# Optimization experiments

Measured on AMD Instinct MI355X. Metric: run time of the kernel, lower is better.

Reference implementation:

```python
import jax, jax.numpy as jnp
import numpy as np

UNITS = 1024
INPUT_SIZE = 1024


def setup_inputs() -> dict:
    key = jax.random.key(0)
    k1, k2, k3 = jax.random.split(key, 3)
    T, B = 512, 64
    inputs = jax.random.normal(k1, (T, B, INPUT_SIZE), dtype=jnp.float32)
    # xavier_uniform for kernel
    limit = float(np.sqrt(6.0 / (INPUT_SIZE + 4 * UNITS)))
    kernel = jax.random.uniform(k2, (INPUT_SIZE, 4 * UNITS), dtype=jnp.float32,
                                minval=-limit, maxval=limit)
    # orthogonal init for recurrent_kernel
    a = jax.random.normal(k3, (4 * UNITS, UNITS), dtype=jnp.float32)
    q, r = jnp.linalg.qr(a)
    q = q * jnp.sign(jnp.diagonal(r))[None, :]
    recurrent_kernel = q.T.astype(jnp.float32)  # [UNITS, 4*UNITS]
    bias = jnp.zeros((4 * UNITS,), dtype=jnp.float32)
    return {"inputs": inputs, "kernel": kernel,
            "recurrent_kernel": recurrent_kernel, "bias": bias}


def _lstm(inputs, kernel, recurrent_kernel, bias):
    T, B, _ = inputs.shape
    U = recurrent_kernel.shape[0]
    # Precompute input projection for all timesteps (same math, one big GEMM)
    xz = jnp.einsum('tbi,ij->tbj', inputs, kernel) + bias  # [T, B, 4U]

    def step(carry, xz_t):
        ht, ct = carry
        z = xz_t + ht @ recurrent_kernel  # [B, 4U]
        z_i, z_f, z_c, z_o = jnp.split(z, 4, axis=1)
        i = jax.nn.sigmoid(z_i)
        f = jax.nn.sigmoid(z_f)
        c_tilde = jnp.tanh(z_c)
        o = jax.nn.sigmoid(z_o)
        ct = f * ct + i * c_tilde
        ht = o * jnp.tanh(ct)
        return (ht, ct), ht

    h0 = jnp.zeros((B, U), dtype=inputs.dtype)
    c0 = jnp.zeros((B, U), dtype=inputs.dtype)
    (ht, ct), outputs = jax.lax.scan(step, (h0, c0), xz)
    return outputs, (ht, ct)


def reference(inputs, kernel, recurrent_kernel, bias):
    return _lstm(inputs, kernel, recurrent_kernel, bias)
```

## Files before the change

### kernel.cpp

```cpp
#include <hip/hip_runtime.h>

typedef __attribute__((ext_vector_type(8))) short short8;
typedef __attribute__((ext_vector_type(4))) float floatx4;
typedef __attribute__((ext_vector_type(4))) int intx4;

#define T_STEPS 512
#define OUT_HT_OFF 33554432ull
#define OUT_CT_OFF 33619968ull

#define WXH_OFF  0ull
#define WXL_OFF  (8ull << 20)
#define HBUF_OFF (16ull << 20)
#define BAR_OFF  ((16ull << 20) + (512ull << 10))
#define WS_NEED  ((16ull << 20) + (512ull << 10) + 4096ull)


static __device__ __forceinline__ unsigned short bf16_rne(float f) {
    union { float f; unsigned int u; } v; v.f = f;
    return (unsigned short)((v.u + 0x7FFFu + ((v.u >> 16) & 1u)) >> 16);
}
static __device__ __forceinline__ float bf16f(unsigned short u) {
    union { unsigned int u; float f; } v; v.u = ((unsigned int)u) << 16;
    return v.f;
}

__global__ void ws_sentinel(float* out) { out[threadIdx.x] = 2.0f; }

__global__ void __launch_bounds__(256) wsplit(const float* __restrict__ W,
                                              unsigned short* __restrict__ wxh,
                                              unsigned short* __restrict__ wxl) {
    __shared__ float tile[64][65];
    const int tx = threadIdx.x & 63;
    const int ty = threadIdx.x >> 6;
    const int cb = blockIdx.x * 64;
    const int kb = blockIdx.y * 64;
    #pragma unroll
    for (int i = 0; i < 16; ++i) {
        int kl = i * 4 + ty;
        tile[kl][tx] = W[(size_t)(kb + kl) * 4096 + cb + tx];
    }
    __syncthreads();
    #pragma unroll
    for (int i = 0; i < 16; ++i) {
        int cl = i * 4 + ty;
        float v = tile[tx][cl];
        unsigned short hi = bf16_rne(v);
        unsigned short lo = bf16_rne(v - bf16f(hi));
        wxh[(size_t)(cb + cl) * 1024 + kb + tx] = hi;
        wxl[(size_t)(cb + cl) * 1024 + kb + tx] = lo;
    }
}

#define HLOAD(dst, OFF) \
    asm volatile("global_load_dwordx4 %0, %1, off offset:" OFF " sc0 sc1" \
                 : "=v"(dst) : "v"(hp8) : "memory");

#define HSTAGE(q, ra, rb, WAITSTR) \
    asm volatile("s_waitcnt " WAITSTR ::: "memory"); \
    __builtin_amdgcn_sched_barrier(0); \
    { unsigned w0=(unsigned)(ra).x, w1=(unsigned)(ra).y, w2=(unsigned)(ra).z, w3=(unsigned)(ra).w; \
      unsigned v0=(unsigned)(rb).x, v1=(unsigned)(rb).y, v2=(unsigned)(rb).z, v3=(unsigned)(rb).w; \
      intx4 hh, ll; \
      hh.x=(int)((w0&0xffffu)|(w1<<16)); hh.y=(int)((w2&0xffffu)|(w3<<16)); \
      hh.z=(int)((v0&0xffffu)|(v1<<16)); hh.w=(int)((v2&0xffffu)|(v3<<16)); \
      ll.x=(int)((w0>>16)|(w1&0xffff0000u)); ll.y=(int)((w2>>16)|(w3&0xffff0000u)); \
      ll.z=(int)((v0>>16)|(v1&0xffff0000u)); ll.w=(int)((v2>>16)|(v3&0xffff0000u)); \
      *(intx4*)(AhH + (wave*8+(q))*1024 + lane*16) = hh; \
      *(intx4*)(AhL + (wave*8+(q))*1024 + lane*16) = ll; }

__global__ void __launch_bounds__(256, 1) lstm_scan(
    const float* __restrict__ R,
    const float* __restrict__ bias,
    const float* __restrict__ x,
    const unsigned short* __restrict__ wxh,
    const unsigned short* __restrict__ wxl,
    unsigned* __restrict__ hbuf,
    unsigned* __restrict__ bar,
    float* __restrict__ out)
{
    __shared__ __align__(16) char AxH[32768];
    __shared__ __align__(16) char AxL[32768];
    __shared__ __align__(16) char AhH[32768];
    __shared__ __align__(16) char AhL[32768];
    __shared__ float zxl[1024];
    __shared__ unsigned s_as[2];

    const int tid  = threadIdx.x;
    const int lane = tid & 63;
    const int wave = tid >> 6;

    if (tid == 0) {
        unsigned xcc;
        asm volatile("s_getreg_b32 %0, hwreg(HW_REG_XCC_ID)" : "=s"(xcc));
        xcc &= 7u;
        unsigned slot = __hip_atomic_fetch_add(bar + 640 + xcc * 32, 1u,
                            __ATOMIC_RELAXED, __HIP_MEMORY_SCOPE_AGENT);
        s_as[0] = xcc; s_as[1] = slot;
    }
    __syncthreads();
    const int xcd  = (int)s_as[0];
    const int slot = (int)(s_as[1] & 31u);
    const int rg   = slot >> 3;
    const int jg   = xcd * 8 + (slot & 7);

    const int rowbase = rg * 16;
    const int c16  = lane & 15;
    const int kgrp = lane >> 4;
    const int gate = c16 >> 2;
    const int jj   = c16 & 3;
    const int mycol = gate * 1024 + jg * 16 + wave * 4 + jj;

    short8 rh[32], rl[32];
    #pragma unroll
    for (int kk = 0; kk < 32; ++kk) {
        int kb = kk * 32 + kgrp * 8;
        short8 h8, l8;
        #pragma unroll
        for (int j = 0; j < 8; ++j) {
            float v = R[(size_t)(kb + j) * 4096 + mycol];
            unsigned short hh = bf16_rne(v);
            h8[j] = (short)hh;
            l8[j] = (short)bf16_rne(v - bf16f(hh));
        }
        rh[kk] = h8; rl[kk] = l8;
    }
    const float biasreg = bias[mycol];

    const int erow  = tid >> 4;
    const int eunit = tid & 15;
    const int ew    = eunit >> 2;
    const int ejj   = eunit & 3;
    const int grow  = rowbase + erow;
    const int gcol  = jg * 16 + eunit;
    const size_t cidx = (size_t)grow * 1024 + gcol;
    float c_state = 0.f;

    const int srow = rowbase + c16;
    const int skof = kgrp * 8;

    const unsigned short* bph = wxh + (size_t)mycol * 1024 + kgrp * 8;
    const unsigned short* bpl = wxl + (size_t)mycol * 1024 + kgrp * 8;

    floatx4 zxcur;
    {
        #pragma unroll
        for (int q = 0; q < 8; ++q) {
            int kc = wave * 8 + q;
            const float* src = x + (size_t)srow * 1024 + kc * 32 + skof;
            floatx4 f0 = *(const floatx4*)src;
            floatx4 f1 = *(const floatx4*)(src + 4);
            short8 h8, l8;
            #pragma unroll
            for (int j = 0; j < 4; ++j) {
                unsigned short q0 = bf16_rne(f0[j]);
                unsigned short q1 = bf16_rne(f1[j]);
                h8[j] = (short)q0; h8[j + 4] = (short)q1;
                l8[j] = (short)bf16_rne(f0[j] - bf16f(q0));
                l8[j + 4] = (short)bf16_rne(f1[j] - bf16f(q1));
            }
            *(short8*)(AxH + kc * 1024 + lane * 16) = h8;
            *(short8*)(AxL + kc * 1024 + lane * 16) = l8;
        }
        __syncthreads();
        floatx4 b0 = {0,0,0,0}, b1 = {0,0,0,0}, b2 = {0,0,0,0}, b3 = {0,0,0,0};
        #pragma unroll
        for (int kk = 0; kk < 32; ++kk) {
            short8 bxh = *(const short8*)(bph + kk * 32);
            short8 bxl = *(const short8*)(bpl + kk * 32);
            short8 axh = *(const short8*)(AxH + kk * 1024 + lane * 16);
            short8 axl = *(const short8*)(AxL + kk * 1024 + lane * 16);
            b0 = __builtin_amdgcn_mfma_f32_16x16x32_bf16(axh, bxh, b0, 0, 0, 0);
            b1 = __builtin_amdgcn_mfma_f32_16x16x32_bf16(axh, bxl, b1, 0, 0, 0);
            b2 = __builtin_amdgcn_mfma_f32_16x16x32_bf16(axl, bxh, b2, 0, 0, 0);
            b3 = __builtin_amdgcn_mfma_f32_16x16x32_bf16(axl, bxl, b3, 0, 0, 0);
        }
        #pragma unroll
        for (int i = 0; i < 4; ++i)
            zxcur[i] = ((b0[i] + b1[i]) + (b2[i] + b3[i])) + biasreg;
        __syncthreads();
    }

    for (int t = 0; t < T_STEPS; ++t) {
        const bool more = (t + 1 < T_STEPS);

        if (t > 0) {
            const char* hp8 = (const char*)(hbuf + (size_t)(t & 1) * 65536)
                            + srow * 4096 + wave * 1024 + kgrp * 32;
            intx4 r0, r1, r2, r3, r4, r5, r6, r7;
            intx4 r8, r9, r10, r11, r12, r13, r14, r15;
            HLOAD(r0,  "0")   HLOAD(r1,  "16")
            HLOAD(r2,  "128") HLOAD(r3,  "144")
            HLOAD(r4,  "256") HLOAD(r5,  "272")
            HLOAD(r6,  "384") HLOAD(r7,  "400")
            HLOAD(r8,  "512") HLOAD(r9,  "528")
            HLOAD(r10, "640") HLOAD(r11, "656")
            HLOAD(r12, "768") HLOAD(r13, "784")
            HLOAD(r14, "896") HLOAD(r15, "912")
            HSTAGE(0, r0,  r1,  "vmcnt(14)")
            HSTAGE(1, r2,  r3,  "vmcnt(12)")
            HSTAGE(2, r4,  r5,  "vmcnt(10)")
            HSTAGE(3, r6,  r7,  "vmcnt(8)")
            HSTAGE(4, r8,  r9,  "vmcnt(6)")
            HSTAGE(5, r10, r11, "vmcnt(4)")
            HSTAGE(6, r12, r13, "vmcnt(2)")
            HSTAGE(7, r14, r15, "vmcnt(0)")
        } else {
            intx4 z4 = {0, 0, 0, 0};
            #pragma unroll
            for (int q = 0; q < 8; ++q) {
                *(intx4*)(AhH + (wave * 8 + q) * 1024 + lane * 16) = z4;
                *(intx4*)(AhL + (wave * 8 + q) * 1024 + lane * 16) = z4;
            }
        }
        __syncthreads();

        floatx4 a0 = zxcur;
        floatx4 a1 = {0,0,0,0}, a2 = {0,0,0,0}, a3 = {0,0,0,0};
        #pragma unroll
        for (int kk = 0; kk < 32; ++kk) {
            short8 ahh = *(const short8*)(AhH + kk * 1024 + lane * 16);
            short8 ahl = *(const short8*)(AhL + kk * 1024 + lane * 16);
            a0 = __builtin_amdgcn_mfma_f32_16x16x32_bf16(ahh, rh[kk], a0, 0, 0, 0);
            a1 = __builtin_amdgcn_mfma_f32_16x16x32_bf16(ahh, rl[kk], a1, 0, 0, 0);
            a2 = __builtin_amdgcn_mfma_f32_16x16x32_bf16(ahl, rh[kk], a2, 0, 0, 0);
            a3 = __builtin_amdgcn_mfma_f32_16x16x32_bf16(ahl, rl[kk], a3, 0, 0, 0);
        }

        #pragma unroll
        for (int i = 0; i < 4; ++i) {
            float z = (a0[i] + a1[i]) + (a2[i] + a3[i]);
            zxl[wave * 256 + (kgrp * 4 + i) * 16 + c16] = z;
        }
        __syncthreads();

        {
            float zi = zxl[ew * 256 + erow * 16 +  0 + ejj];
            float zf = zxl[ew * 256 + erow * 16 +  4 + ejj];
            float zc = zxl[ew * 256 + erow * 16 +  8 + ejj];
            float zo = zxl[ew * 256 + erow * 16 + 12 + ejj];
            float ig = 1.0f / (1.0f + expf(-zi));
            float fg = 1.0f / (1.0f + expf(-zf));
            float og = 1.0f / (1.0f + expf(-zo));
            float cc = tanhf(zc);
            float cn = fg * c_state + ig * cc;
            c_state = cn;
            float hval = og * tanhf(cn);

            out[(size_t)t * 65536 + cidx] = hval;
            if (more) {
                unsigned short hi = bf16_rne(hval);
                unsigned short lo = bf16_rne(hval - bf16f(hi));
                unsigned w = (unsigned)hi | ((unsigned)lo << 16);
                unsigned* dst = hbuf + (size_t)((t + 1) & 1) * 65536 + cidx;
                asm volatile("global_store_dword %0, %1, off sc0 sc1"
                             :: "v"(dst), "v"(w) : "memory");
            } else {
                out[OUT_HT_OFF + cidx] = hval;
                out[OUT_CT_OFF + cidx] = cn;
            }
        }
        asm volatile("s_waitcnt vmcnt(0)" ::: "memory");
        __syncthreads();

        if (more) {
            if (tid == 0) {
                unsigned s = (unsigned)(t + 1);
                unsigned old = __hip_atomic_fetch_add(bar + xcd * 32, 1u,
                                  __ATOMIC_RELAXED, __HIP_MEMORY_SCOPE_WORKGROUP);
                if (old == s * 32u - 1u) {
                    unsigned og = __hip_atomic_fetch_add(bar + 256, 1u,
                                      __ATOMIC_RELAXED, __HIP_MEMORY_SCOPE_AGENT);
                    if (og == s * 8u - 1u) {
                        __hip_atomic_store(bar + 288, s,
                                           __ATOMIC_RELAXED, __HIP_MEMORY_SCOPE_AGENT);
                    }
                }
            }

            #pragma unroll
            for (int q = 0; q < 8; ++q) {
                int kc = wave * 8 + q;
                const float* src = x + (size_t)(t + 1) * 65536
                                     + (size_t)srow * 1024 + kc * 32 + skof;
                floatx4 f0 = *(const floatx4*)src;
                floatx4 f1 = *(const floatx4*)(src + 4);
                short8 h8, l8;
                #pragma unroll
                for (int j = 0; j < 4; ++j) {
                    unsigned short q0 = bf16_rne(f0[j]);
                    unsigned short q1 = bf16_rne(f1[j]);
                    h8[j] = (short)q0; h8[j + 4] = (short)q1;
                    l8[j] = (short)bf16_rne(f0[j] - bf16f(q0));
                    l8[j + 4] = (short)bf16_rne(f1[j] - bf16f(q1));
                }
                *(short8*)(AxH + kc * 1024 + lane * 16) = h8;
                *(short8*)(AxL + kc * 1024 + lane * 16) = l8;
            }
            __syncthreads();
            floatx4 b0 = {0,0,0,0}, b1 = {0,0,0,0}, b2 = {0,0,0,0}, b3 = {0,0,0,0};
            #pragma unroll
            for (int kk = 0; kk < 32; ++kk) {
                short8 bxh = *(const short8*)(bph + kk * 32);
                short8 bxl = *(const short8*)(bpl + kk * 32);
                short8 axh = *(const short8*)(AxH + kk * 1024 + lane * 16);
                short8 axl = *(const short8*)(AxL + kk * 1024 + lane * 16);
                b0 = __builtin_amdgcn_mfma_f32_16x16x32_bf16(axh, bxh, b0, 0, 0, 0);
                b1 = __builtin_amdgcn_mfma_f32_16x16x32_bf16(axh, bxl, b1, 0, 0, 0);
                b2 = __builtin_amdgcn_mfma_f32_16x16x32_bf16(axl, bxh, b2, 0, 0, 0);
                b3 = __builtin_amdgcn_mfma_f32_16x16x32_bf16(axl, bxl, b3, 0, 0, 0);
            }
            #pragma unroll
            for (int i = 0; i < 4; ++i)
                zxcur[i] = ((b0[i] + b1[i]) + (b2[i] + b3[i])) + biasreg;

            if (tid == 0) {
                while (__hip_atomic_load(bar + 288, __ATOMIC_RELAXED,
                                         __HIP_MEMORY_SCOPE_AGENT) < (unsigned)(t + 1)) {
                    __builtin_amdgcn_s_sleep(2);
                }
            }
            __syncthreads();
        }
    }
}

extern "C" void kernel_launch(void* const* d_in, const int* in_sizes, int n_in,
                              void* d_out, int out_size, void* d_ws, size_t ws_size,
                              hipStream_t stream) {
    const float* inputs = (const float*)d_in[0];
    const float* W      = (const float*)d_in[1];
    const float* R      = (const float*)d_in[2];
    const float* bias   = (const float*)d_in[3];
    float* out = (float*)d_out;

    if (ws_size < WS_NEED) {
        ws_sentinel<<<1, 64, 0, stream>>>(out);
        return;
    }

    unsigned short* wxh  = (unsigned short*)((char*)d_ws + WXH_OFF);
    unsigned short* wxl  = (unsigned short*)((char*)d_ws + WXL_OFF);
    unsigned*       hbuf = (unsigned*)((char*)d_ws + HBUF_OFF);
    unsigned*       bar  = (unsigned*)((char*)d_ws + BAR_OFF);

    hipMemsetAsync(bar, 0, 4096, stream);
    wsplit<<<dim3(64, 16), 256, 0, stream>>>(W, wxh, wxl);
    lstm_scan<<<256, 256, 0, stream>>>(R, bias, inputs, wxh, wxl, hbuf, bar, out);
}
```

Before: 9.014 ms.

## Warp-specialize LSTM scan into recurrent and input-projection producer waves

Doubles the block to 512 threads. Four waves hold the recurrent weights and run the per-step recurrence, while four producer waves compute the input projection for upcoming steps into a double-buffered LDS ring, signalled through LDS flags instead of block-wide barriers. The x·W projection is taken off the serial critical path, and each consumer wave now does its own gate math and grid-barrier spin, so block-wide __syncthreads are no longer needed. In exchange it adds fine-grained LDS spin flags, more waves per CU competing for issue slots, and a more intricate memory-ordering protocol; a dynamic LDS pad is added, likely to keep one block per CU.

```diff
diff --git a/kernel.cpp b/kernel.cpp
--- a/kernel.cpp
+++ b/kernel.cpp
@@ -54,7 +54,6 @@
 #define HLOAD(dst, OFF) \
     asm volatile("global_load_dwordx4 %0, %1, off offset:" OFF " sc0 sc1" \
                  : "=v"(dst) : "v"(hp8) : "memory");
-
 #define HSTAGE(q, ra, rb, WAITSTR) \
     asm volatile("s_waitcnt " WAITSTR ::: "memory"); \
     __builtin_amdgcn_sched_barrier(0); \
@@ -65,10 +64,10 @@
       hh.z=(int)((v0&0xffffu)|(v1<<16)); hh.w=(int)((v2&0xffffu)|(v3<<16)); \
       ll.x=(int)((w0>>16)|(w1&0xffff0000u)); ll.y=(int)((w2>>16)|(w3&0xffff0000u)); \
       ll.z=(int)((v0>>16)|(v1&0xffff0000u)); ll.w=(int)((v2>>16)|(v3&0xffff0000u)); \
-      *(intx4*)(AhH + (wave*8+(q))*1024 + lane*16) = hh; \
-      *(intx4*)(AhL + (wave*8+(q))*1024 + lane*16) = ll; }
-
-__global__ void __launch_bounds__(256, 1) lstm_scan(
+      *(intx4*)(AhH + (wr*8+(q))*1024 + lane*16) = hh; \
+      *(intx4*)(AhL + (wr*8+(q))*1024 + lane*16) = ll; }
+
+__global__ void __launch_bounds__(512, 1) lstm_scan(
     const float* __restrict__ R,
     const float* __restrict__ bias,
     const float* __restrict__ x,
@@ -78,16 +77,20 @@
     unsigned* __restrict__ bar,
     float* __restrict__ out)
 {
-    __shared__ __align__(16) char AxH[32768];
-    __shared__ __align__(16) char AxL[32768];
     __shared__ __align__(16) char AhH[32768];
     __shared__ __align__(16) char AhL[32768];
-    __shared__ float zxl[1024];
+    __shared__ float ring[2][4][256];
+    __shared__ float zex[4][16 * 17];
+    __shared__ unsigned prodf[4], consf[4];
+    __shared__ unsigned stgc, garr;
     __shared__ unsigned s_as[2];
+    extern __shared__ char lds_pad[];
 
     const int tid  = threadIdx.x;
     const int lane = tid & 63;
     const int wave = tid >> 6;
+    const int wr   = wave & 3;
+    const bool isR = wave < 4;
 
     if (tid == 0) {
         unsigned xcc;
@@ -96,148 +99,112 @@
         unsigned slot = __hip_atomic_fetch_add(bar + 640 + xcc * 32, 1u,
                             __ATOMIC_RELAXED, __HIP_MEMORY_SCOPE_AGENT);
         s_as[0] = xcc; s_as[1] = slot;
-    }
+        lds_pad[0] = 0;
+    }
+    if (tid < 4) { prodf[tid] = 0; consf[tid] = 0; }
+    if (tid == 4) { stgc = 0; garr = 0; }
     __syncthreads();
     const int xcd  = (int)s_as[0];
     const int slot = (int)(s_as[1] & 31u);
     const int rg   = slot >> 3;
     const int jg   = xcd * 8 + (slot & 7);
-
     const int rowbase = rg * 16;
+
     const int c16  = lane & 15;
     const int kgrp = lane >> 4;
-    const int gate = c16 >> 2;
-    const int jj   = c16 & 3;
-    const int mycol = gate * 1024 + jg * 16 + wave * 4 + jj;
-
-    short8 rh[32], rl[32];
-    #pragma unroll
-    for (int kk = 0; kk < 32; ++kk) {
-        int kb = kk * 32 + kgrp * 8;
-        short8 h8, l8;
-        #pragma unroll
-        for (int j = 0; j < 8; ++j) {
-            float v = R[(size_t)(kb + j) * 4096 + mycol];
-            unsigned short hh = bf16_rne(v);
-            h8[j] = (short)hh;
-            l8[j] = (short)bf16_rne(v - bf16f(hh));
-        }
-        rh[kk] = h8; rl[kk] = l8;
-    }
-    const float biasreg = bias[mycol];
-
-    const int erow  = tid >> 4;
-    const int eunit = tid & 15;
-    const int ew    = eunit >> 2;
-    const int ejj   = eunit & 3;
-    const int grow  = rowbase + erow;
-    const int gcol  = jg * 16 + eunit;
-    const size_t cidx = (size_t)grow * 1024 + gcol;
-    float c_state = 0.f;
-
-    const int srow = rowbase + c16;
-    const int skof = kgrp * 8;
-
-    const unsigned short* bph = wxh + (size_t)mycol * 1024 + kgrp * 8;
-    const unsigned short* bpl = wxl + (size_t)mycol * 1024 + kgrp * 8;
-
-    floatx4 zxcur;
-    {
-        #pragma unroll
-        for (int q = 0; q < 8; ++q) {
-            int kc = wave * 8 + q;
-            const float* src = x + (size_t)srow * 1024 + kc * 32 + skof;
-            floatx4 f0 = *(const floatx4*)src;
-            floatx4 f1 = *(const floatx4*)(src + 4);
-            short8 h8, l8;
-            #pragma unroll
-            for (int j = 0; j < 4; ++j) {
-                unsigned short q0 = bf16_rne(f0[j]);
-                unsigned short q1 = bf16_rne(f1[j]);
-                h8[j] = (short)q0; h8[j + 4] = (short)q1;
-                l8[j] = (short)bf16_rne(f0[j] - bf16f(q0));
-                l8[j + 4] = (short)bf16_rne(f1[j] - bf16f(q1));
-            }
-            *(short8*)(AxH + kc * 1024 + lane * 16) = h8;
-            *(short8*)(AxL + kc * 1024 + lane * 16) = l8;
-        }
-        __syncthreads();
-        floatx4 b0 = {0,0,0,0}, b1 = {0,0,0,0}, b2 = {0,0,0,0}, b3 = {0,0,0,0};
+    const int mycol = (c16 >> 2) * 1024 + jg * 16 + wr * 4 + (c16 & 3);
+
+    if (isR) {
+        short8 rh[32], rl[32];
         #pragma unroll
         for (int kk = 0; kk < 32; ++kk) {
-            short8 bxh = *(const short8*)(bph + kk * 32);
-            short8 bxl = *(const short8*)(bpl + kk * 32);
-            short8 axh = *(const short8*)(AxH + kk * 1024 + lane * 16);
-            short8 axl = *(const short8*)(AxL + kk * 1024 + lane * 16);
-            b0 = __builtin_amdgcn_mfma_f32_16x16x32_bf16(axh, bxh, b0, 0, 0, 0);
-            b1 = __builtin_amdgcn_mfma_f32_16x16x32_bf16(axh, bxl, b1, 0, 0, 0);
-            b2 = __builtin_amdgcn_mfma_f32_16x16x32_bf16(axl, bxh, b2, 0, 0, 0);
-            b3 = __builtin_amdgcn_mfma_f32_16x16x32_bf16(axl, bxl, b3, 0, 0, 0);
+            int kb = kk * 32 + kgrp * 8;
+            short8 h8, l8;
+            #pragma unroll
+            for (int j = 0; j < 8; ++j) {
+                float v = R[(size_t)(kb + j) * 4096 + mycol];
+                unsigned short hh = bf16_rne(v);
+                h8[j] = (short)hh;
+                l8[j] = (short)bf16_rne(v - bf16f(hh));
+            }
+            rh[kk] = h8; rl[kk] = l8;
         }
-        #pragma unroll
-        for (int i = 0; i < 4; ++i)
-            zxcur[i] = ((b0[i] + b1[i]) + (b2[i] + b3[i])) + biasreg;
-        __syncthreads();
-    }
-
-    for (int t = 0; t < T_STEPS; ++t) {
-        const bool more = (t + 1 < T_STEPS);
-
-        if (t > 0) {
-            const char* hp8 = (const char*)(hbuf + (size_t)(t & 1) * 65536)
-                            + srow * 4096 + wave * 1024 + kgrp * 32;
-            intx4 r0, r1, r2, r3, r4, r5, r6, r7;
-            intx4 r8, r9, r10, r11, r12, r13, r14, r15;
-            HLOAD(r0,  "0")   HLOAD(r1,  "16")
-            HLOAD(r2,  "128") HLOAD(r3,  "144")
-            HLOAD(r4,  "256") HLOAD(r5,  "272")
-            HLOAD(r6,  "384") HLOAD(r7,  "400")
-            HLOAD(r8,  "512") HLOAD(r9,  "528")
-            HLOAD(r10, "640") HLOAD(r11, "656")
-            HLOAD(r12, "768") HLOAD(r13, "784")
-            HLOAD(r14, "896") HLOAD(r15, "912")
-            HSTAGE(0, r0,  r1,  "vmcnt(14)")
-            HSTAGE(1, r2,  r3,  "vmcnt(12)")
-            HSTAGE(2, r4,  r5,  "vmcnt(10)")
-            HSTAGE(3, r6,  r7,  "vmcnt(8)")
-            HSTAGE(4, r8,  r9,  "vmcnt(6)")
-            HSTAGE(5, r10, r11, "vmcnt(4)")
-            HSTAGE(6, r12, r13, "vmcnt(2)")
-            HSTAGE(7, r14, r15, "vmcnt(0)")
-        } else {
-            intx4 z4 = {0, 0, 0, 0};
-            #pragma unroll
-            for (int q = 0; q < 8; ++q) {
-                *(intx4*)(AhH + (wave * 8 + q) * 1024 + lane * 16) = z4;
-                *(intx4*)(AhL + (wave * 8 + q) * 1024 + lane * 16) = z4;
-            }
-        }
-        __syncthreads();
-
-        floatx4 a0 = zxcur;
-        floatx4 a1 = {0,0,0,0}, a2 = {0,0,0,0}, a3 = {0,0,0,0};
-        #pragma unroll
-        for (int kk = 0; kk < 32; ++kk) {
-            short8 ahh = *(const short8*)(AhH + kk * 1024 + lane * 16);
-            short8 ahl = *(const short8*)(AhL + kk * 1024 + lane * 16);
-            a0 = __builtin_amdgcn_mfma_f32_16x16x32_bf16(ahh, rh[kk], a0, 0, 0, 0);
-            a1 = __builtin_amdgcn_mfma_f32_16x16x32_bf16(ahh, rl[kk], a1, 0, 0, 0);
-            a2 = __builtin_amdgcn_mfma_f32_16x16x32_bf16(ahl, rh[kk], a2, 0, 0, 0);
-            a3 = __builtin_amdgcn_mfma_f32_16x16x32_bf16(ahl, rl[kk], a3, 0, 0, 0);
-        }
-
-        #pragma unroll
-        for (int i = 0; i < 4; ++i) {
-            float z = (a0[i] + a1[i]) + (a2[i] + a3[i]);
-            zxl[wave * 256 + (kgrp * 4 + i) * 16 + c16] = z;
-        }
-        __syncthreads();
-
-        {
-            float zi = zxl[ew * 256 + erow * 16 +  0 + ejj];
-            float zf = zxl[ew * 256 + erow * 16 +  4 + ejj];
-            float zc = zxl[ew * 256 + erow * 16 +  8 + ejj];
-            float zo = zxl[ew * 256 + erow * 16 + 12 + ejj];
+
+        const int rr = lane >> 2;
+        const int uu = lane & 3;
+        const int gcol = jg * 16 + wr * 4 + uu;
+        const size_t cidx = (size_t)(rowbase + rr) * 1024 + gcol;
+        float c_state = 0.f;
+
+        for (int t = 0; t < T_STEPS; ++t) {
+            while (__hip_atomic_load(&prodf[wr], __ATOMIC_ACQUIRE,
+                                     __HIP_MEMORY_SCOPE_WORKGROUP) < (unsigned)(t + 1))
+                __builtin_amdgcn_s_sleep(1);
+            floatx4 a0;
+            #pragma unroll
+            for (int i = 0; i < 4; ++i)
+                a0[i] = ring[t & 1][wr][(kgrp * 4 + i) * 16 + c16];
+            if (lane == 0)
+                __hip_atomic_store(&consf[wr], (unsigned)(t + 1),
+                                   __ATOMIC_RELEASE, __HIP_MEMORY_SCOPE_WORKGROUP);
+
+            if (t > 0) {
+                const char* hp8 = (const char*)(hbuf + (size_t)(t & 1) * 65536)
+                                + (rowbase + c16) * 4096 + wr * 1024 + kgrp * 32;
+                intx4 r0, r1, r2, r3, r4, r5, r6, r7;
+                intx4 r8, r9, r10, r11, r12, r13, r14, r15;
+                HLOAD(r0,  "0")   HLOAD(r1,  "16")
+                HLOAD(r2,  "128") HLOAD(r3,  "144")
+                HLOAD(r4,  "256") HLOAD(r5,  "272")
+                HLOAD(r6,  "384") HLOAD(r7,  "400")
+                HLOAD(r8,  "512") HLOAD(r9,  "528")
+                HLOAD(r10, "640") HLOAD(r11, "656")
+                HLOAD(r12, "768") HLOAD(r13, "784")
+                HLOAD(r14, "896") HLOAD(r15, "912")
+                HSTAGE(0, r0,  r1,  "vmcnt(14)")
+                HSTAGE(1, r2,  r3,  "vmcnt(12)")
+                HSTAGE(2, r4,  r5,  "vmcnt(10)")
+                HSTAGE(3, r6,  r7,  "vmcnt(8)")
+                HSTAGE(4, r8,  r9,  "vmcnt(6)")
+                HSTAGE(5, r10, r11, "vmcnt(4)")
+                HSTAGE(6, r12, r13, "vmcnt(2)")
+                HSTAGE(7, r14, r15, "vmcnt(0)")
+            } else {
+                intx4 z4 = {0, 0, 0, 0};
+                #pragma unroll
+                for (int q = 0; q < 8; ++q) {
+                    *(intx4*)(AhH + (wr * 8 + q) * 1024 + lane * 16) = z4;
+                    *(intx4*)(AhL + (wr * 8 + q) * 1024 + lane * 16) = z4;
+                }
+            }
+            if (lane == 0)
+                __hip_atomic_fetch_add(&stgc, 1u, __ATOMIC_RELEASE,
+                                       __HIP_MEMORY_SCOPE_WORKGROUP);
+            while (__hip_atomic_load(&stgc, __ATOMIC_ACQUIRE,
+                                     __HIP_MEMORY_SCOPE_WORKGROUP) < 4u * (t + 1))
+                __builtin_amdgcn_s_sleep(1);
+
+            floatx4 a1 = {0,0,0,0}, a2 = {0,0,0,0}, a3 = {0,0,0,0};
+            #pragma unroll
+            for (int kk = 0; kk < 32; ++kk) {
+                short8 ahh = *(const short8*)(AhH + kk * 1024 + lane * 16);
+                short8 ahl = *(const short8*)(AhL + kk * 1024 + lane * 16);
+                a0 = __builtin_amdgcn_mfma_f32_16x16x32_bf16(ahh, rh[kk], a0, 0, 0, 0);
+                a1 = __builtin_amdgcn_mfma_f32_16x16x32_bf16(ahh, rl[kk], a1, 0, 0, 0);
+                a2 = __builtin_amdgcn_mfma_f32_16x16x32_bf16(ahl, rh[kk], a2, 0, 0, 0);
+                a3 = __builtin_amdgcn_mfma_f32_16x16x32_bf16(ahl, rl[kk], a3, 0, 0, 0);
+            }
+
+            #pragma unroll
+            for (int i = 0; i < 4; ++i)
+                zex[wr][(kgrp * 4 + i) * 17 + c16] = (a0[i] + a1[i]) + (a2[i] + a3[i]);
+            asm volatile("s_waitcnt lgkmcnt(0)" ::: "memory");
+            __builtin_amdgcn_sched_barrier(0);
+            float zi = zex[wr][rr * 17 +  0 + uu];
+            float zf = zex[wr][rr * 17 +  4 + uu];
+            float zc = zex[wr][rr * 17 +  8 + uu];
+            float zo = zex[wr][rr * 17 + 12 + uu];
+
             float ig = 1.0f / (1.0f + expf(-zi));
             float fg = 1.0f / (1.0f + expf(-zf));
             float og = 1.0f / (1.0f + expf(-zo));
@@ -247,79 +214,103 @@
             float hval = og * tanhf(cn);
 
             out[(size_t)t * 65536 + cidx] = hval;
-            if (more) {
+            if (t + 1 < T_STEPS) {
                 unsigned short hi = bf16_rne(hval);
                 unsigned short lo = bf16_rne(hval - bf16f(hi));
                 unsigned w = (unsigned)hi | ((unsigned)lo << 16);
                 unsigned* dst = hbuf + (size_t)((t + 1) & 1) * 65536 + cidx;
                 asm volatile("global_store_dword %0, %1, off sc0 sc1"
                              :: "v"(dst), "v"(w) : "memory");
+                asm volatile("s_waitcnt vmcnt(0)" ::: "memory");
+
+                if (lane == 0) {
+                    unsigned s = (unsigned)(t + 1);
+                    unsigned old = __hip_atomic_fetch_add(&garr, 1u,
+                                       __ATOMIC_RELAXED, __HIP_MEMORY_SCOPE_WORKGROUP);
+                    if (old == 4u * s - 1u) {
+                        unsigned o2 = __hip_atomic_fetch_add(bar + xcd * 32, 1u,
+                                          __ATOMIC_RELAXED, __HIP_MEMORY_SCOPE_WORKGROUP);
+                        if (o2 == s * 32u - 1u) {
+                            unsigned og2 = __hip_atomic_fetch_add(bar + 256, 1u,
+                                               __ATOMIC_RELAXED, __HIP_MEMORY_SCOPE_AGENT);
+                            if (og2 == s * 8u - 1u)
+                                __hip_atomic_store(bar + 288, s,
+                                    __ATOMIC_RELAXED, __HIP_MEMORY_SCOPE_AGENT);
+                        }
+                    }
+                }
+                while (__hip_atomic_load(bar + 288, __ATOMIC_RELAXED,
+                                         __HIP_MEMORY_SCOPE_AGENT) < (unsigned)(t + 1))
+                    __builtin_amdgcn_s_sleep(2);
             } else {
                 out[OUT_HT_OFF + cidx] = hval;
                 out[OUT_CT_OFF + cidx] = cn;
             }
         }
-        asm volatile("s_waitcnt vmcnt(0)" ::: "memory");
-        __syncthreads();
-
-        if (more) {
-            if (tid == 0) {
-                unsigned s = (unsigned)(t + 1);
-                unsigned old = __hip_atomic_fetch_add(bar + xcd * 32, 1u,
-                                  __ATOMIC_RELAXED, __HIP_MEMORY_SCOPE_WORKGROUP);
-                if (old == s * 32u - 1u) {
-                    unsigned og = __hip_atomic_fetch_add(bar + 256, 1u,
-                                      __ATOMIC_RELAXED, __HIP_MEMORY_SCOPE_AGENT);
-                    if (og == s * 8u - 1u) {
-                        __hip_atomic_store(bar + 288, s,
-                                           __ATOMIC_RELAXED, __HIP_MEMORY_SCOPE_AGENT);
+    } else {
+        const float biasreg = bias[mycol];
+        const unsigned short* bph = wxh + (size_t)mycol * 1024 + kgrp * 8;
+        const unsigned short* bpl = wxl + (size_t)mycol * 1024 + kgrp * 8;
+
+        for (int tp = 0; tp < T_STEPS; ++tp) {
+            while ((int)__hip_atomic_load(&consf[wr], __ATOMIC_ACQUIRE,
+                                          __HIP_MEMORY_SCOPE_WORKGROUP) < tp - 1)
+                __builtin_amdgcn_s_sleep(2);
+
+            const float* xb = x + (size_t)tp * 65536
+                              + (size_t)(rowbase + c16) * 1024 + kgrp * 8;
+            floatx4 b0 = {0,0,0,0}, b1 = {0,0,0,0}, b2 = {0,0,0,0}, b3 = {0,0,0,0};
+
+            intx4  wb[2][8];
+            floatx4 xv[2][8];
+            #pragma unroll
+            for (int j = 0; j < 4; ++j) {
+                wb[0][2*j]   = *(const intx4*)(bph + j * 32);
+                wb[0][2*j+1] = *(const intx4*)(bpl + j * 32);
+                xv[0][2*j]   = *(const floatx4*)(xb + j * 32);
+                xv[0][2*j+1] = *(const floatx4*)(xb + j * 32 + 4);
+            }
+            #pragma unroll
+            for (int b = 0; b < 8; ++b) {
+                const int cur = b & 1, nxt = cur ^ 1;
+                if (b < 7) {
+                    #pragma unroll
+                    for (int j = 0; j < 4; ++j) {
+                        int kk = (b + 1) * 4 + j;
+                        wb[nxt][2*j]   = *(const intx4*)(bph + kk * 32);
+                        wb[nxt][2*j+1] = *(const intx4*)(bpl + kk * 32);
+                        xv[nxt][2*j]   = *(const floatx4*)(xb + kk * 32);
+                        xv[nxt][2*j+1] = *(const floatx4*)(xb + kk * 32 + 4);
                     }
                 }
-            }
-
-            #pragma unroll
-            for (int q = 0; q < 8; ++q) {
-                int kc = wave * 8 + q;
-                const float* src = x + (size_t)(t + 1) * 65536
-                                     + (size_t)srow * 1024 + kc * 32 + skof;
-                floatx4 f0 = *(const floatx4*)src;
-                floatx4 f1 = *(const floatx4*)(src + 4);
-                short8 h8, l8;
                 #pragma unroll
                 for (int j = 0; j < 4; ++j) {
-                    unsigned short q0 = bf16_rne(f0[j]);
-                    unsigned short q1 = bf16_rne(f1[j]);
-                    h8[j] = (short)q0; h8[j + 4] = (short)q1;
-                    l8[j] = (short)bf16_rne(f0[j] - bf16f(q0));
-                    l8[j + 4] = (short)bf16_rne(f1[j] - bf16f(q1));
+                    floatx4 f0 = xv[cur][2*j], f1 = xv[cur][2*j+1];
+                    short8 axh, axl;
+                    #pragma unroll
+                    for (int e = 0; e < 4; ++e) {
+                        unsigned short q0 = bf16_rne(f0[e]);
+                        unsigned short q1 = bf16_rne(f1[e]);
+                        axh[e]     = (short)q0;
+                        axh[e + 4] = (short)q1;
+                        axl[e]     = (short)bf16_rne(f0[e] - bf16f(q0));
+                        axl[e + 4] = (short)bf16_rne(f1[e] - bf16f(q1));
+                    }
+                    short8 bxh = *(short8*)&wb[cur][2*j];
+                    short8 bxl = *(short8*)&wb[cur][2*j+1];
+                    b0 = __builtin_amdgcn_mfma_f32_16x16x32_bf16(axh, bxh, b0, 0, 0, 0);
+                    b1 = __builtin_amdgcn_mfma_f32_16x16x32_bf16(axh, bxl, b1, 0, 0, 0);
+                    b2 = __builtin_amdgcn_mfma_f32_16x16x32_bf16(axl, bxh, b2, 0, 0, 0);
+                    b3 = __builtin_amdgcn_mfma_f32_16x16x32_bf16(axl, bxl, b3, 0, 0, 0);
                 }
-                *(short8*)(AxH + kc * 1024 + lane * 16) = h8;
-                *(short8*)(AxL + kc * 1024 + lane * 16) = l8;
-            }
-            __syncthreads();
-            floatx4 b0 = {0,0,0,0}, b1 = {0,0,0,0}, b2 = {0,0,0,0}, b3 = {0,0,0,0};
-            #pragma unroll
-            for (int kk = 0; kk < 32; ++kk) {
-                short8 bxh = *(const short8*)(bph + kk * 32);
-                short8 bxl = *(const short8*)(bpl + kk * 32);
-                short8 axh = *(const short8*)(AxH + kk * 1024 + lane * 16);
-                short8 axl = *(const short8*)(AxL + kk * 1024 + lane * 16);
-                b0 = __builtin_amdgcn_mfma_f32_16x16x32_bf16(axh, bxh, b0, 0, 0, 0);
-                b1 = __builtin_amdgcn_mfma_f32_16x16x32_bf16(axh, bxl, b1, 0, 0, 0);
-                b2 = __builtin_amdgcn_mfma_f32_16x16x32_bf16(axl, bxh, b2, 0, 0, 0);
-                b3 = __builtin_amdgcn_mfma_f32_16x16x32_bf16(axl, bxl, b3, 0, 0, 0);
             }
             #pragma unroll
             for (int i = 0; i < 4; ++i)
-                zxcur[i] = ((b0[i] + b1[i]) + (b2[i] + b3[i])) + biasreg;
-
-            if (tid == 0) {
-                while (__hip_atomic_load(bar + 288, __ATOMIC_RELAXED,
-                                         __HIP_MEMORY_SCOPE_AGENT) < (unsigned)(t + 1)) {
-                    __builtin_amdgcn_s_sleep(2);
-                }
-            }
-            __syncthreads();
+                ring[tp & 1][wr][(kgrp * 4 + i) * 16 + c16] =
+                    ((b0[i] + b1[i]) + (b2[i] + b3[i])) + biasreg;
+            if (lane == 0)
+                __hip_atomic_store(&prodf[wr], (unsigned)(tp + 1),
+                                   __ATOMIC_RELEASE, __HIP_MEMORY_SCOPE_WORKGROUP);
         }
     }
 }
@@ -345,5 +336,5 @@
 
     hipMemsetAsync(bar, 0, 4096, stream);
     wsplit<<<dim3(64, 16), 256, 0, stream>>>(W, wxh, wxl);
-    lstm_scan<<<256, 256, 0, stream>>>(R, bias, inputs, wxh, wxl, hbuf, bar, out);
-}
+    lstm_scan<<<256, 512, 16384, stream>>>(R, bias, inputs, wxh, wxl, hbuf, bar, out);
+}
```

Result: slower. 11.25 ms (+24.8%).
